# Kernel tuning notes

Hardware: AMD Instinct MI355X
Metric: run time of the kernel (lower is better)

Reference implementation:

```python
import jax, jax.numpy as jnp
import numpy as np

BN_EPS = 1e-5


def fps(xyz, npoint):
    # farthest point sampling; xyz: (B,N,3) -> (B,npoint) int32, starts at index 0 (torch convention)
    B, N, _ = xyz.shape
    def step(carry, _):
        dist, last = carry
        lp = jnp.take_along_axis(xyz, last[:, None, None], axis=1)  # (B,1,3)
        d = jnp.sum((xyz - lp) ** 2, -1)                             # (B,N)
        dist = jnp.minimum(dist, d)
        nxt = jnp.argmax(dist, -1).astype(jnp.int32)
        return (dist, nxt), nxt
    init = (jnp.full((B, N), 1e10, xyz.dtype), jnp.zeros((B,), jnp.int32))
    _, rest = jax.lax.scan(step, init, None, length=npoint - 1)
    return jnp.concatenate([jnp.zeros((1, B), jnp.int32), rest], 0).T  # (B,npoint)


def knn_idx(xyz, centers, k):
    # xyz (B,N,3), centers (B,S,3) -> (B,S,k) nearest-neighbor indices
    d = (jnp.sum(centers ** 2, -1)[:, :, None]
         + jnp.sum(xyz ** 2, -1)[:, None, :]
         - 2.0 * jnp.einsum('bsc,bnc->bsn', centers, xyz))
    _, idx = jax.lax.top_k(-d, k)
    return idx


def group(feat, idx):
    # feat (B,N,C), idx (B,S,K) -> (B,S,K,C)
    return jax.vmap(lambda f, i: f[i])(feat, idx)


def sa_knn(xyz, points, npoint, nsample, w1, b1, w2, b2):
    # xyz (B,N,3), points (B,N,C); returns new_xyz (B,S,3), new_points (B,S,Cout)
    fidx = fps(xyz, npoint)
    new_xyz = jnp.take_along_axis(xyz, fidx[:, :, None], axis=1)        # (B,S,3)
    idx = knn_idx(xyz, new_xyz, nsample)                                 # (B,S,K)
    g_xyz = group(xyz, idx) - new_xyz[:, :, None, :]                     # relative coords
    g_pts = group(points, idx)
    x = jnp.concatenate([g_xyz, g_pts], -1)                              # (B,S,K,3+C)
    x = jax.nn.relu(jnp.einsum('bskc,oc->bsko', x, w1) + b1)
    x = jnp.einsum('bskc,oc->bsko', x, w2) + b2                          # last conv: no activation
    return new_xyz, jnp.max(x, 2)                                        # max over neighbors


def sa_all(xyz, points, w1, b1, w2, b2):
    # group_all: concat xyz+points over all N, shared MLP, max over N -> (B,Cout)
    x = jnp.concatenate([xyz, points], -1)                               # (B,N,3+C)
    x = jax.nn.relu(jnp.einsum('bnc,oc->bno', x, w1) + b1)
    x = jnp.einsum('bnc,oc->bno', x, w2) + b2
    return jnp.max(x, 1)


def fc_head(x, w1, b1, g1, be1, w2, b2, g2, be2):
    # Linear + BN(eval, running mean=0/var=1) + ReLU, twice; Dropout = identity in eval
    s = 1.0 / np.sqrt(1.0 + BN_EPS)
    x = jax.nn.relu(g1 * ((x @ w1.T + b1) * s) + be1)
    x = jax.nn.relu(g2 * ((x @ w2.T + b2) * s) + be2)
    return x


def forward(point_cloud, sa1_w1, sa1_b1, sa1_w2, sa1_b2,
            sa2_w1, sa2_b1, sa2_w2, sa2_b2,
            sa3_w1, sa3_b1, sa3_w2, sa3_b2,
            fc_w1, fc_b1, fc_g1, fc_be1, fc_w2, fc_b2, fc_g2, fc_be2):
    xyz = jnp.transpose(point_cloud, (0, 2, 1))  # (B,N,3)
    nsamples2 = (16, 32, 48)
    logits, codes = [], []
    for i in range(3):  # three structurally distinct branches
        x1, p1 = sa_knn(xyz, xyz, 512, 16, sa1_w1[i], sa1_b1[i], sa1_w2[i], sa1_b2[i])
        x2, p2 = sa_knn(x1, p1, 128, nsamples2[i], sa2_w1[i], sa2_b1[i], sa2_w2[i], sa2_b2[i])
        code = sa_all(x2, p2, sa3_w1[i], sa3_b1[i], sa3_w2[i], sa3_b2[i])   # (B,512)
        logits.append(fc_head(code, fc_w1[i], fc_b1[i], fc_g1[i], fc_be1[i],
                              fc_w2[i], fc_b2[i], fc_g2[i], fc_be2[i]))      # (B,128)
        codes.append(code)
    return tuple(logits) + tuple(codes)


def setup_inputs():
    key = jax.random.key(0)
    ks = iter(jax.random.split(key, 16))
    def w(shape, s=0.05):
        return jax.random.normal(next(ks), shape, jnp.float32) * s
    B, N = 32, 2048
    inp = {'point_cloud': jax.random.normal(next(ks), (B, 3, N), jnp.float32)}
    inp.update(
        sa1_w1=w((3, 64, 6)), sa1_b1=jnp.zeros((3, 64)), sa1_w2=w((3, 128, 64)), sa1_b2=jnp.zeros((3, 128)),
        sa2_w1=w((3, 128, 131)), sa2_b1=jnp.zeros((3, 128)), sa2_w2=w((3, 256, 128)), sa2_b2=jnp.zeros((3, 256)),
        sa3_w1=w((3, 512, 259)), sa3_b1=jnp.zeros((3, 512)), sa3_w2=w((3, 512, 512)), sa3_b2=jnp.zeros((3, 512)),
        fc_w1=w((3, 256, 512)), fc_b1=jnp.zeros((3, 256)), fc_g1=jnp.ones((3, 256)), fc_be1=jnp.zeros((3, 256)),
        fc_w2=w((3, 128, 256)), fc_b2=jnp.zeros((3, 128)), fc_g2=jnp.ones((3, 128)), fc_be2=jnp.zeros((3, 128)),
    )
    return inp


def reference(point_cloud, sa1_w1, sa1_b1, sa1_w2, sa1_b2,
              sa2_w1, sa2_b1, sa2_w2, sa2_b2,
              sa3_w1, sa3_b1, sa3_w2, sa3_b2,
              fc_w1, fc_b1, fc_g1, fc_be1, fc_w2, fc_b2, fc_g2, fc_be2):
    return forward(point_cloud, sa1_w1, sa1_b1, sa1_w2, sa1_b2,
                   sa2_w1, sa2_b1, sa2_w2, sa2_b2,
                   sa3_w1, sa3_b1, sa3_w2, sa3_b2,
                   fc_w1, fc_b1, fc_g1, fc_be1, fc_w2, fc_b2, fc_g2, fc_be2)
```

## Files before the change

### kernel.cpp

```cpp
#include <hip/hip_runtime.h>
#include <hip/hip_bf16.h>
#include <math.h>

#define DEVI __device__ __forceinline__

static constexpr int BB = 32, NN = 2048, S1 = 512, S2 = 128;

typedef float f32x4 __attribute__((ext_vector_type(4)));
typedef short s16x8 __attribute__((ext_vector_type(8)));

static constexpr size_t OFF_XS   = 0;
static constexpr size_t OFF_YS   = OFF_XS + (size_t)BB*NN;
static constexpr size_t OFF_ZS   = OFF_YS + (size_t)BB*NN;
static constexpr size_t OFF_SSQ  = OFF_ZS + (size_t)BB*NN;
static constexpr size_t OFF_NX1X = OFF_SSQ + (size_t)BB*NN;
static constexpr size_t OFF_NX1Y = OFF_NX1X + (size_t)BB*S1;
static constexpr size_t OFF_NX1Z = OFF_NX1Y + (size_t)BB*S1;
static constexpr size_t OFF_NX2X = OFF_NX1Z + (size_t)BB*S1;
static constexpr size_t OFF_NX2Y = OFF_NX2X + (size_t)BB*S2;
static constexpr size_t OFF_NX2Z = OFF_NX2Y + (size_t)BB*S2;
static constexpr size_t OFF_CODE = OFF_NX2Z + (size_t)BB*S2;
static constexpr size_t OFF_O3P  = OFF_CODE + (size_t)3*BB*512;
static constexpr size_t OFF_P1   = OFF_O3P + (size_t)3*BB*4*512;
static constexpr size_t OFF_X3   = OFF_P1 + (size_t)3*BB*S1*128;
static constexpr size_t OFF_H3   = OFF_X3 + (size_t)3*BB*S2*260;
static constexpr size_t OFF_W    = OFF_H3 + (size_t)3*BB*S2*512;
static constexpr size_t W1A  = OFF_W;
static constexpr size_t B1A  = W1A + 3*64*6;
static constexpr size_t W2A  = B1A + 3*64;
static constexpr size_t B2A  = W2A + 3*128*64;
static constexpr size_t W1B  = B2A + 3*128;
static constexpr size_t B1B  = W1B + 3*128*132;
static constexpr size_t W2B  = B1B + 3*128;
static constexpr size_t B2B  = W2B + 3*256*128;
static constexpr size_t W1C  = B2B + 3*256;
static constexpr size_t B1C  = W1C + 3*512*260;
static constexpr size_t W2C  = B1C + 3*512;
static constexpr size_t B2C  = W2C + 3*512*512;
static constexpr size_t FW1  = B2C + 3*512;
static constexpr size_t FB1  = FW1 + 3*256*512;
static constexpr size_t FG1  = FB1 + 3*256;
static constexpr size_t FBE1 = FG1 + 3*256;
static constexpr size_t FW2  = FBE1 + 3*256;
static constexpr size_t FB2  = FW2 + 3*128*256;
static constexpr size_t FG2  = FB2 + 3*128;
static constexpr size_t FBE2 = FG2 + 3*128;
static constexpr size_t OFF_KNN1 = FBE2 + 3*128;
static constexpr size_t OFF_KNN2 = OFF_KNN1 + (size_t)BB*S1*16;
static constexpr size_t OFF_W1BF = OFF_KNN2 + (size_t)BB*S2*48;
static constexpr size_t OFF_W2BF = OFF_W1BF + 30720;
static constexpr size_t OFF_W1CBH = OFF_W2BF + 49152;
static constexpr size_t OFF_W1CBL = OFF_W1CBH + 221184;
static constexpr size_t OFF_W2CBH = OFF_W1CBL + 221184;
static constexpr size_t OFF_W2CBL = OFF_W2CBH + 393216;
static constexpr size_t OFF_X3BH  = OFF_W2CBL + 393216;
static constexpr size_t OFF_X3BL  = OFF_X3BH + 1769472;
static constexpr size_t OFF_H3BH  = OFF_X3BL + 1769472;
static constexpr size_t OFF_H3BL  = OFF_H3BH + 3145728;
static constexpr size_t OFF_W2ABH = OFF_H3BL + 3145728;
static constexpr size_t OFF_W2ABL = OFF_W2ABH + 12288;
static constexpr size_t WS_FLOATS = OFF_W2ABL + 12288;

__device__ __align__(16) float g_ws[WS_FLOATS];
__device__ int g_is_f32;
__device__ int g_flip;
__device__ int g_bad;
__device__ int g_nz;

DEVI float bf2f(const __hip_bfloat16 v){ return __bfloat162float(v); }
DEVI float rn_add(float a, float b){ return __fadd_rn(a,b); }
DEVI float rn_mul(float a, float b){ return __fmul_rn(a,b); }
DEVI float rn_sub(float a, float b){ return __fsub_rn(a,b); }
DEVI float sq3(float x,float y,float z){ return rn_add(rn_add(rn_mul(x,x),rn_mul(y,y)),rn_mul(z,z)); }

DEVI float ldany(const void* s, size_t i, int isf){
  return isf ? ((const float*)s)[i] : bf2f(((const __hip_bfloat16*)s)[i]);
}
DEVI unsigned short f2bf(float f){
  unsigned u = __float_as_uint(f);
  unsigned r = (u + 0x7FFFu + ((u>>16)&1u)) >> 16;
  return (unsigned short)r;
}
DEVI float bfbits2f(unsigned short h){ return __uint_as_float(((unsigned)h)<<16); }
DEVI void mfma16(f32x4& d, s16x8 a, s16x8 b){
  asm volatile("v_mfma_f32_16x16x32_bf16 %0, %1, %2, %0" : "+v"(d) : "v"(a), "v"(b));
}
DEVI void mfma_guard(f32x4& d){
  asm volatile("s_nop 7\n\ts_nop 7\n\ts_nop 2" : "+v"(d));
}

#define DPPF(dst, src, CTRL) dst = __uint_as_float((unsigned)__builtin_amdgcn_update_dpp(\
    (int)__float_as_uint(src), (int)__float_as_uint(src), CTRL, 0xF, 0xF, false))
#define DPPI(dst, src, CTRL) dst = __builtin_amdgcn_update_dpp(src, src, CTRL, 0xF, 0xF, false)
#define RED_STEP(CTRL) { float ov; int oi; DPPF(ov, best, CTRL); DPPI(oi, bidx, CTRL); \
  if (ov > best || (ov == best && oi < bidx)){ best = ov; bidx = oi; } }
#define WAVE_ARGMAX() RED_STEP(0xB1) RED_STEP(0x4E) RED_STEP(0x124) RED_STEP(0x128) RED_STEP(0x142) RED_STEP(0x143)

#define REDMIN_STEP(CTRL) { float ov; int oi; DPPF(ov, best, CTRL); DPPI(oi, bidx, CTRL); \
  if (ov < best || (ov == best && oi < bidx)){ best = ov; bidx = oi; } }
#define WAVE_ARGMIN() REDMIN_STEP(0xB1) REDMIN_STEP(0x4E) REDMIN_STEP(0x124) REDMIN_STEP(0x128) REDMIN_STEP(0x142) REDMIN_STEP(0x143)

__global__ __launch_bounds__(256) void init_detect_kernel(const void* __restrict__ pc){
  __shared__ int s_cnt[256];
  int t = threadIdx.x;
  if (t==0){ g_flip=0; g_bad=0; g_nz=0; }
  const unsigned short* h = (const unsigned short*)pc;
  int weird = 0;
  for (int i=t; i<4096; i+=256){
    unsigned short v = h[2*i];
    int e = (v >> 7) & 0xFF;
    if (e == 0xFF || e < 90 || e > 140) weird++;
  }
  s_cnt[t] = weird; __syncthreads();
  for (int o=128;o>0;o>>=1){ if (t<o) s_cnt[t]+=s_cnt[t+o]; __syncthreads(); }
  if (t==0) g_is_f32 = (s_cnt[0] > 1024) ? 1 : 0;
}

struct ParamPtrs { const void* p[20]; };

DEVI void cvt_arr(const void* s, float* d, int n, int g, int gs, int isf){
  for (int i=g;i<n;i+=gs) d[i] = ldany(s,i,isf);
}
DEVI void cvt_pad(const void* s, float* d, int rows, int cin, int cinp, int g, int gs, int isf){
  int tot = rows*cinp;
  for (int i=g;i<tot;i+=gs){ int r=i/cinp, c=i%cinp; d[i] = (c<cin)? ldany(s,(size_t)r*cin+c,isf) : 0.f; }
}

__global__ __launch_bounds__(256) void cvtprep_kernel(ParamPtrs pp, const void* __restrict__ pc, int mode){
  if (mode==1 && g_flip==0) return;
  const int isf = g_is_f32 ^ mode;
  if (blockIdx.x < 256){
    int i = blockIdx.x*256 + threadIdx.x;
    int b = i >> 11, n = i & 2047;
    float x = ldany(pc, (size_t)(b*3+0)*2048 + n, isf);
    float y = ldany(pc, (size_t)(b*3+1)*2048 + n, isf);
    float z = ldany(pc, (size_t)(b*3+2)*2048 + n, isf);
    g_ws[OFF_XS+i]=x; g_ws[OFF_YS+i]=y; g_ws[OFF_ZS+i]=z;
    g_ws[OFF_SSQ+i]=sq3(x,y,z);
    return;
  }
  int g = (blockIdx.x-256)*256 + threadIdx.x; int gs = 512*256;
  float* ws = g_ws;
  cvt_arr(pp.p[0],  ws+W1A, 3*64*6, g, gs, isf);
  cvt_arr(pp.p[1],  ws+B1A, 3*64, g, gs, isf);
  cvt_arr(pp.p[2],  ws+W2A, 3*128*64, g, gs, isf);
  cvt_arr(pp.p[3],  ws+B2A, 3*128, g, gs, isf);
  cvt_pad(pp.p[4],  ws+W1B, 3*128, 131, 132, g, gs, isf);
  cvt_arr(pp.p[5],  ws+B1B, 3*128, g, gs, isf);
  cvt_arr(pp.p[6],  ws+W2B, 3*256*128, g, gs, isf);
  cvt_arr(pp.p[7],  ws+B2B, 3*256, g, gs, isf);
  cvt_pad(pp.p[8],  ws+W1C, 3*512, 259, 260, g, gs, isf);
  cvt_arr(pp.p[9],  ws+B1C, 3*512, g, gs, isf);
  cvt_arr(pp.p[10], ws+W2C, 3*512*512, g, gs, isf);
  cvt_arr(pp.p[11], ws+B2C, 3*512, g, gs, isf);
  cvt_arr(pp.p[12], ws+FW1, 3*256*512, g, gs, isf);
  cvt_arr(pp.p[13], ws+FB1, 3*256, g, gs, isf);
  cvt_arr(pp.p[14], ws+FG1, 3*256, g, gs, isf);
  cvt_arr(pp.p[15], ws+FBE1,3*256, g, gs, isf);
  cvt_arr(pp.p[16], ws+FW2, 3*128*256, g, gs, isf);
  cvt_arr(pp.p[17], ws+FB2, 3*128, g, gs, isf);
  cvt_arr(pp.p[18], ws+FG2, 3*128, g, gs, isf);
  cvt_arr(pp.p[19], ws+FBE2,3*128, g, gs, isf);
}

__global__ __launch_bounds__(256) void scan_check_kernel(){
  size_t off; int n, g, gs;
  if (blockIdx.x < 128){ off = OFF_XS; n = 3*BB*NN; g = blockIdx.x*256 + threadIdx.x; gs = 128*256; }
  else { off = FW1; n = 3*256*512; g = (blockIdx.x-128)*256 + threadIdx.x; gs = 128*256; }
  int bad=0, nz=0;
  for (int i=g;i<n;i+=gs){
    float v = g_ws[off + i];
    if (v != v || fabsf(v) > 1e4f) bad=1;
    if (fabsf(v) > 1e-20f) nz=1;
  }
  unsigned long long mb = __ballot(bad), mn = __ballot(nz);
  if ((threadIdx.x & 63)==0){
    if (mb) atomicOr(&g_bad, 1);
    if (mn) atomicOr(&g_nz, 1);
  }
}

__global__ __launch_bounds__(64) void resolve_flip_kernel(){
  if (threadIdx.x==0){
    g_flip = (g_bad || !g_nz) ? 1 : 0;
    g_bad = 0; g_nz = 0;
  }
}

DEVI void cvt_bf16_body(int g, int gs){
  unsigned short* w1d = (unsigned short*)(g_ws + OFF_W1BF);
  for (int i=g; i<3*128*160; i+=gs){
    int br = i/(128*160); int rem = i%(128*160); int h = rem/160; int c = rem%160;
    float v = (c<132) ? g_ws[W1B + ((size_t)br*128 + h)*132 + c] : 0.f;
    w1d[i] = f2bf(v);
  }
  unsigned short* w2d = (unsigned short*)(g_ws + OFF_W2BF);
  for (int i=g; i<3*256*128; i+=gs) w2d[i] = f2bf(g_ws[W2B + i]);
  unsigned short* w1ch = (unsigned short*)(g_ws + OFF_W1CBH);
  unsigned short* w1cl = (unsigned short*)(g_ws + OFF_W1CBL);
  for (int i=g; i<3*512*288; i+=gs){
    int br = i/(512*288); int rem = i%(512*288); int n = rem/288; int c = rem%288;
    float v = (c<260) ? g_ws[W1C + ((size_t)br*512 + n)*260 + c] : 0.f;
    unsigned short hi = f2bf(v);
    w1ch[i] = hi; w1cl[i] = f2bf(v - bfbits2f(hi));
  }
  unsigned short* w2ch = (unsigned short*)(g_ws + OFF_W2CBH);
  unsigned short* w2cl = (unsigned short*)(g_ws + OFF_W2CBL);
  for (int i=g; i<3*512*512; i+=gs){
    float v = g_ws[W2C + i];
    unsigned short hi = f2bf(v);
    w2ch[i] = hi; w2cl[i] = f2bf(v - bfbits2f(hi));
  }
  unsigned short* w2ah = (unsigned short*)(g_ws + OFF_W2ABH);
  unsigned short* w2al = (unsigned short*)(g_ws + OFF_W2ABL);
  for (int i=g; i<3*128*64; i+=gs){
    float v = g_ws[W2A + i];
    unsigned short hi = f2bf(v);
    w2ah[i] = hi; w2al[i] = f2bf(v - bfbits2f(hi));
  }
}

#define FPS_DECL(J) float px##J, py##J, pz##J, dd##J;
#define FPS_LD256A(J) { int n=(J)*256+t; px##J=xs[n]; py##J=ys[n]; pz##J=zs[n]; dd##J=1e10f; xl[n]=px##J; yl[n]=py##J; zl[n]=pz##J; }
#define FPS_LD256B(J) { int n=(J)*256+t; px##J=xs[n]; py##J=ys[n]; pz##J=zs[n]; dd##J=ddg[n]; xl[n]=px##J; yl[n]=py##J; zl[n]=pz##J; }
#define FPS_SAVE(J) ddg[(J)*256+t]=dd##J;
#define FPS_LD64(J) { int n=(J)*64+t; px##J=xs[n]; py##J=ys[n]; pz##J=zs[n]; dd##J=1e10f; xl[n]=px##J; yl[n]=py##J; zl[n]=pz##J; }
#define FPS_UPD(J) { float dx=rn_sub(px##J,lx), dy=rn_sub(py##J,ly), dz=rn_sub(pz##J,lz); float d=sq3(dx,dy,dz); dd##J=fminf(dd##J,d); }
#define FPS_T1(J,JA,JB) float v##J; int q##J; { bool c = dd##JB > dd##JA; v##J = c? dd##JB : dd##JA; q##J = c? (JB) : (JA); }
#define FPS_T2(JA,JB) { bool c = v##JB > v##JA; v##JA = c? v##JB : v##JA; q##JA = c? q##JB : q##JA; }

#define FPS1_ITER_BODY() \
    FPS_UPD(0) FPS_UPD(1) FPS_UPD(2) FPS_UPD(3) FPS_UPD(4) FPS_UPD(5) FPS_UPD(6) FPS_UPD(7) \
    FPS_T1(0,0,1) FPS_T1(1,2,3) FPS_T1(2,4,5) FPS_T1(3,6,7) \
    FPS_T2(0,1) FPS_T2(2,3) \
    FPS_T2(0,2) \
    float best = v0; int bidx = q0*256 + t; \
    WAVE_ARGMAX() \
    int par = i & 1; \
    if ((t&63)==63){ s_val[par][wave]=best; s_idx[par][wave]=bidx; } \
    __syncthreads(); \
    float va = s_val[par][0], vb = s_val[par][1], vc = s_val[par][2], vd = s_val[par][3]; \
    int ia = s_idx[par][0], ib = s_idx[par][1], ic = s_idx[par][2], id_ = s_idx[par][3]; \
    if (vb > va || (vb == va && ib < ia)){ va = vb; ia = ib; } \
    if (vd > vc || (vd == vc && id_ < ic)){ vc = vd; ic = id_; } \
    if (vc > va || (vc == va && ic < ia)){ va = vc; ia = ic; } \
    int gidx = ia; \
    lx = xl[gidx]; ly = yl[gidx]; lz = zl[gidx]; \
    if (t==0){ nx[i]=lx; ny[i]=ly; nz[i]=lz; }

__global__ __launch_bounds__(256,1) void fps1a_cvt_kernel(){
  const int t = threadIdx.x;
  if (blockIdx.x >= 32){
    cvt_bf16_body((blockIdx.x-32)*256 + t, 256*256);
    return;
  }
  const int b = blockIdx.x;
  const int wave = t >> 6;
  const float* xs = g_ws + OFF_XS + (size_t)b*NN;
  const float* ys = g_ws + OFF_YS + (size_t)b*NN;
  const float* zs = g_ws + OFF_ZS + (size_t)b*NN;
  float* nx = g_ws + OFF_NX1X + (size_t)b*S1;
  float* ny = g_ws + OFF_NX1Y + (size_t)b*S1;
  float* nz = g_ws + OFF_NX1Z + (size_t)b*S1;
  float* ddg = g_ws + OFF_X3 + (size_t)b*NN;
  __shared__ float xl[NN], yl[NN], zl[NN];
  __shared__ float s_val[2][4]; __shared__ int s_idx[2][4];
  FPS_DECL(0) FPS_DECL(1) FPS_DECL(2) FPS_DECL(3) FPS_DECL(4) FPS_DECL(5) FPS_DECL(6) FPS_DECL(7)
  FPS_LD256A(0) FPS_LD256A(1) FPS_LD256A(2) FPS_LD256A(3) FPS_LD256A(4) FPS_LD256A(5) FPS_LD256A(6) FPS_LD256A(7)
  __syncthreads();
  float lx = xl[0], ly = yl[0], lz = zl[0];
  if (t==0){ nx[0]=lx; ny[0]=ly; nz[0]=lz; }
  for (int i=1;i<256;i++){
    FPS1_ITER_BODY()
  }
  FPS_SAVE(0) FPS_SAVE(1) FPS_SAVE(2) FPS_SAVE(3) FPS_SAVE(4) FPS_SAVE(5) FPS_SAVE(6) FPS_SAVE(7)
}

#define KNN1_POISON(C) case C: d[C] = match ? 3.0e38f : d[C]; break;
DEVI void knn1_body(int wid, int lane){
  int b = wid >> 9;
  const float* xs = g_ws + OFF_XS + (size_t)b*NN;
  const float* ys = g_ws + OFF_YS + (size_t)b*NN;
  const float* zs = g_ws + OFF_ZS + (size_t)b*NN;
  const float* sq = g_ws + OFF_SSQ + (size_t)b*NN;
  float cx = g_ws[OFF_NX1X + wid], cy = g_ws[OFF_NX1Y + wid], cz = g_ws[OFF_NX1Z + wid];
  float sc = sq3(cx,cy,cz);
  float d[32];
  #pragma unroll
  for (int c=0;c<32;c++){
    int n = c*64 + lane;
    float x=xs[n], y=ys[n], z=zs[n];
    float dot = rn_add(rn_add(rn_mul(cx,x),rn_mul(cy,y)),rn_mul(cz,z));
    d[c] = rn_sub(rn_add(sc,sq[n]), rn_mul(2.f,dot));
  }
  int* out = (int*)(g_ws + OFF_KNN1) + (size_t)wid*16;
  for (int r=0;r<16;r++){
    float tv[16]; int tc[16];
    #pragma unroll
    for (int c=0;c<16;c++){
      float a = d[2*c];
      float e = d[2*c+1];
      bool cc = e < a;
      tv[c] = cc ? e : a; tc[c] = cc ? (2*c+1) : (2*c);
    }
    #pragma unroll
    for (int s=1; s<16; s<<=1){
      #pragma unroll
      for (int c=0;c<16;c+=2){
        if ((c % (2*s)) == 0 && c+s < 16){
          bool cc = tv[c+s] < tv[c];
          tv[c] = cc ? tv[c+s] : tv[c];
          tc[c] = cc ? tc[c+s] : tc[c];
        }
      }
    }
    float best = tv[0]; int bidx = tc[0]*64 + lane;
    WAVE_ARGMIN()
    int wbi = __builtin_amdgcn_readlane(bidx, 63);
    if (lane == 0) out[r] = wbi;
    bool match = (lane == (wbi & 63));
    switch ((wbi >> 6) & 31){
      KNN1_POISON(0)  KNN1_POISON(1)  KNN1_POISON(2)  KNN1_POISON(3)
      KNN1_POISON(4)  KNN1_POISON(5)  KNN1_POISON(6)  KNN1_POISON(7)
      KNN1_POISON(8)  KNN1_POISON(9)  KNN1_POISON(10) KNN1_POISON(11)
      KNN1_POISON(12) KNN1_POISON(13) KNN1_POISON(14) KNN1_POISON(15)
      KNN1_POISON(16) KNN1_POISON(17) KNN1_POISON(18) KNN1_POISON(19)
      KNN1_POISON(20) KNN1_POISON(21) KNN1_POISON(22) KNN1_POISON(23)
      KNN1_POISON(24) KNN1_POISON(25) KNN1_POISON(26) KNN1_POISON(27)
      KNN1_POISON(28) KNN1_POISON(29) KNN1_POISON(30) KNN1_POISON(31)
    }
  }
}

__global__ __launch_bounds__(256,1) void fps1b_knn1a_kernel(){
  const int t = threadIdx.x;
  if (blockIdx.x >= 32){
    int lin = ((blockIdx.x-32)*256 + t) >> 6;
    int b = lin >> 8, s = lin & 255;
    knn1_body(b*S1 + s, t & 63);
    return;
  }
  const int b = blockIdx.x;
  const int wave = t >> 6;
  const float* xs = g_ws + OFF_XS + (size_t)b*NN;
  const float* ys = g_ws + OFF_YS + (size_t)b*NN;
  const float* zs = g_ws + OFF_ZS + (size_t)b*NN;
  float* nx = g_ws + OFF_NX1X + (size_t)b*S1;
  float* ny = g_ws + OFF_NX1Y + (size_t)b*S1;
  float* nz = g_ws + OFF_NX1Z + (size_t)b*S1;
  const float* ddg = g_ws + OFF_X3 + (size_t)b*NN;
  __shared__ float xl[NN], yl[NN], zl[NN];
  __shared__ float s_val[2][4]; __shared__ int s_idx[2][4];
  FPS_DECL(0) FPS_DECL(1) FPS_DECL(2) FPS_DECL(3) FPS_DECL(4) FPS_DECL(5) FPS_DECL(6) FPS_DECL(7)
  FPS_LD256B(0) FPS_LD256B(1) FPS_LD256B(2) FPS_LD256B(3) FPS_LD256B(4) FPS_LD256B(5) FPS_LD256B(6) FPS_LD256B(7)
  __syncthreads();
  float lx = nx[255], ly = ny[255], lz = nz[255];
  for (int i=256;i<S1;i++){
    FPS1_ITER_BODY()
  }
}

__global__ __launch_bounds__(256) void fps2_knn1b_kernel(){
  if (blockIdx.x >= 32){
    int lin = ((blockIdx.x-32)*256 + threadIdx.x) >> 6;
    int b = lin >> 8, s = lin & 255;
    knn1_body(b*S1 + 256 + s, threadIdx.x & 63);
    return;
  }
  if (threadIdx.x >= 64) return;
  const int b = blockIdx.x, t = threadIdx.x;
  const float* xs = g_ws + OFF_NX1X + (size_t)b*S1;
  const float* ys = g_ws + OFF_NX1Y + (size_t)b*S1;
  const float* zs = g_ws + OFF_NX1Z + (size_t)b*S1;
  float* nx = g_ws + OFF_NX2X + (size_t)b*S2;
  float* ny = g_ws + OFF_NX2Y + (size_t)b*S2;
  float* nz = g_ws + OFF_NX2Z + (size_t)b*S2;
  __shared__ float xl[S1], yl[S1], zl[S1];
  FPS_DECL(0) FPS_DECL(1) FPS_DECL(2) FPS_DECL(3) FPS_DECL(4) FPS_DECL(5) FPS_DECL(6) FPS_DECL(7)
  FPS_LD64(0) FPS_LD64(1) FPS_LD64(2) FPS_LD64(3) FPS_LD64(4) FPS_LD64(5) FPS_LD64(6) FPS_LD64(7)
  float lx = xl[0], ly = yl[0], lz = zl[0];
  if (t==0){ nx[0]=lx; ny[0]=ly; nz[0]=lz; }
  for (int i=1;i<S2;i++){
    FPS_UPD(0) FPS_UPD(1) FPS_UPD(2) FPS_UPD(3) FPS_UPD(4) FPS_UPD(5) FPS_UPD(6) FPS_UPD(7)
    FPS_T1(0,0,1) FPS_T1(1,2,3) FPS_T1(2,4,5) FPS_T1(3,6,7)
    FPS_T2(0,1) FPS_T2(2,3)
    FPS_T2(0,2)
    float best = v0; int bidx = q0*64 + t;
    WAVE_ARGMAX()
    int gidx = __builtin_amdgcn_readlane(bidx, 63);
    lx = xl[gidx]; ly = yl[gidx]; lz = zl[gidx];
    if (t==0){ nx[i]=lx; ny[i]=ly; nz[i]=lz; }
  }
}

#define KNN2_POISON(C) case C: d[C] = match ? 3.0e38f : d[C]; break;
DEVI void knn2_body(int wid, int lane){
  int b = wid >> 7;
  const float* xs = g_ws + OFF_NX1X + (size_t)b*S1;
  const float* ys = g_ws + OFF_NX1Y + (size_t)b*S1;
  const float* zs = g_ws + OFF_NX1Z + (size_t)b*S1;
  float cx = g_ws[OFF_NX2X + wid], cy = g_ws[OFF_NX2Y + wid], cz = g_ws[OFF_NX2Z + wid];
  float sc = sq3(cx,cy,cz);
  float d[8];
  #pragma unroll
  for (int c=0;c<8;c++){
    int n = c*64 + lane;
    float x=xs[n], y=ys[n], z=zs[n];
    float sx = sq3(x,y,z);
    float dot = rn_add(rn_add(rn_mul(cx,x),rn_mul(cy,y)),rn_mul(cz,z));
    d[c] = rn_sub(rn_add(sc,sx), rn_mul(2.f,dot));
  }
  int* out = (int*)(g_ws + OFF_KNN2) + (size_t)wid*48;
  for (int r=0;r<48;r++){
    float tv[4]; int tc[4];
    #pragma unroll
    for (int c=0;c<4;c++){
      float a = d[2*c];
      float e = d[2*c+1];
      bool cc = e < a;
      tv[c] = cc ? e : a; tc[c] = cc ? (2*c+1) : (2*c);
    }
    { bool cc = tv[1] < tv[0]; tv[0] = cc?tv[1]:tv[0]; tc[0] = cc?tc[1]:tc[0]; }
    { bool cc = tv[3] < tv[2]; tv[2] = cc?tv[3]:tv[2]; tc[2] = cc?tc[3]:tc[2]; }
    { bool cc = tv[2] < tv[0]; tv[0] = cc?tv[2]:tv[0]; tc[0] = cc?tc[2]:tc[0]; }
    float best = tv[0]; int bidx = tc[0]*64 + lane;
    WAVE_ARGMIN()
    int wbi = __builtin_amdgcn_readlane(bidx, 63);
    if (lane == 0) out[r] = wbi;
    bool match = (lane == (wbi & 63));
    switch ((wbi >> 6) & 7){
      KNN2_POISON(0) KNN2_POISON(1) KNN2_POISON(2) KNN2_POISON(3)
      KNN2_POISON(4) KNN2_POISON(5) KNN2_POISON(6) KNN2_POISON(7)
    }
  }
}

__global__ __launch_bounds__(256) void knn2_sa1_kernel(){
  const int t = threadIdx.x;
  if (blockIdx.x < 1024){
    knn2_body((blockIdx.x*256 + t) >> 6, t & 63);
    return;
  }
  const int bx2 = blockIdx.x - 1024;
  const int br = bx2 >> 10;
  const int bxx = bx2 & 1023;
  const int wave = t>>6, lane = t&63, quad = lane>>4, l16 = lane&15;
  __shared__ float w1s[384];
  __shared__ float b1s[64];
  __shared__ __align__(16) short Hh[4][16*72];
  __shared__ __align__(16) short Hl[4][16*72];
  for (int i=t;i<384;i+=256) w1s[i] = g_ws[W1A + (size_t)br*384 + i];
  if (t<64) b1s[t] = g_ws[B1A + br*64 + t];
  __syncthreads();
  const int* kn = (const int*)(g_ws + OFF_KNN1);
  const short* w2h = (const short*)(g_ws + OFF_W2ABH) + (size_t)br*128*64;
  const short* w2l = (const short*)(g_ws + OFF_W2ABL) + (size_t)br*128*64;
  const float* b2 = g_ws + B2A + br*128;
  for (int it=0; it<4; it++){
    int gid = bxx*16 + it*4 + wave;
    int b = gid >> 9;
    int idx = kn[(size_t)gid*16 + l16] & (NN-1);
    float cx = g_ws[OFF_NX1X+gid], cy = g_ws[OFF_NX1Y+gid], cz = g_ws[OFF_NX1Z+gid];
    size_t gl = (size_t)b*NN + idx;
    float x = g_ws[OFF_XS+gl], y = g_ws[OFF_YS+gl], z = g_ws[OFF_ZS+gl];
    float f0=x-cx, f1=y-cy, f2=z-cz;
    #pragma unroll
    for (int i=0;i<16;i++){
      int h = quad*16 + i;
      float acc = b1s[h];
      acc += f0*w1s[h*6+0] + f1*w1s[h*6+1] + f2*w1s[h*6+2]
           +  x*w1s[h*6+3] +  y*w1s[h*6+4] +  z*w1s[h*6+5];
      acc = fmaxf(acc, 0.f);
      unsigned short hi = f2bf(acc);
      Hh[wave][l16*72 + h] = (short)hi;
      Hl[wave][l16*72 + h] = (short)f2bf(acc - bfbits2f(hi));
    }
    s16x8 ah[2], al[2];
    #pragma unroll
    for (int ks=0;ks<2;ks++){
      ah[ks] = *(const s16x8*)(&Hh[wave][l16*72 + ks*32 + quad*8]);
      al[ks] = *(const s16x8*)(&Hl[wave][l16*72 + ks*32 + quad*8]);
    }
    unsigned short* P1g = (unsigned short*)(g_ws + OFF_P1) + ((size_t)br*16384 + gid)*128;
    #pragma unroll
    for (int ni=0; ni<8; ni++){
      int o = ni*16 + l16;
      f32x4 acc = {0.f,0.f,0.f,0.f};
      #pragma unroll
      for (int ks=0; ks<2; ks++){
        s16x8 bh = *(const s16x8*)(w2h + (size_t)o*64 + ks*32 + quad*8);
        s16x8 bl = *(const s16x8*)(w2l + (size_t)o*64 + ks*32 + quad*8);
        mfma16(acc, ah[ks], bh);
        mfma16(acc, ah[ks], bl);
        mfma16(acc, al[ks], bh);
      }
      mfma_guard(acc);
      float vmax = fmaxf(fmaxf(acc[0],acc[1]), fmaxf(acc[2],acc[3]));
      vmax = fmaxf(vmax, __shfl_xor(vmax,16));
      vmax = fmaxf(vmax, __shfl_xor(vmax,32));
      if (quad==0) P1g[o] = f2bf(vmax + b2[o]);
    }
  }
}

template<int K>
DEVI void sa2_body(int br, int g2, short* Xb, short* Hb, float* ctr, int* idxs){
  constexpr int MT = K/16;
  const int b = g2 >> 7;
  const int t = threadIdx.x;
  const int wave = t >> 6, lane = t & 63, quad = lane >> 4, l16 = lane & 15;
  const int* kn2 = (const int*)(g_ws + OFF_KNN2) + (size_t)g2*48;
  if (t < K) idxs[t] = kn2[t] & (S1-1);
  if (t < 3) ctr[t] = g_ws[(t==0?OFF_NX2X:(t==1?OFF_NX2Y:OFF_NX2Z)) + g2];
  __syncthreads();
  const unsigned short* p1b = (const unsigned short*)(g_ws + OFF_P1) + (size_t)br*16384*128;
  const int grp = t >> 5, gl = t & 31;
  for (int k = grp; k < K; k += 8){
    int idx = idxs[k];
    const unsigned short* row = p1b + ((size_t)b*S1 + idx)*128;
    unsigned long long w = *(const unsigned long long*)(row + gl*4);
    short* dst = &Xb[k*168 + 3 + gl*4];
    dst[0] = (short)(w & 0xFFFF);
    dst[1] = (short)((w >> 16) & 0xFFFF);
    dst[2] = (short)((w >> 32) & 0xFFFF);
    dst[3] = (short)((w >> 48) & 0xFFFF);
    if (gl < 32) Xb[k*168 + 131 + gl] = 0;
    if (gl < 5)  Xb[k*168 + 163 + gl] = 0;
  }
  if (t < K){
    int idx = idxs[t];
    float c0 = g_ws[OFF_NX1X + (size_t)b*S1 + idx] - ctr[0];
    float c1 = g_ws[OFF_NX1Y + (size_t)b*S1 + idx] - ctr[1];
    float c2 = g_ws[OFF_NX1Z + (size_t)b*S1 + idx] - ctr[2];
    Xb[t*168+0] = (short)f2bf(c0);
    Xb[t*168+1] = (short)f2bf(c1);
    Xb[t*168+2] = (short)f2bf(c2);
  }
  __syncthreads();
  {
    const short* w1bf = (const short*)(g_ws + OFF_W1BF) + (size_t)br*128*160;
    const float* b1 = g_ws + B1B + br*128;
    for (int ni = wave; ni < 8; ni += 4){
      int h = ni*16 + l16;
      s16x8 bfr[5];
      #pragma unroll
      for (int ks=0;ks<5;ks++) bfr[ks] = *(const s16x8*)(w1bf + (size_t)h*160 + ks*32 + quad*8);
      float bias = b1[h];
      #pragma unroll
      for (int m=0; m<MT; m++){
        f32x4 acc = {0.f,0.f,0.f,0.f};
        #pragma unroll
        for (int ks=0;ks<5;ks++){
          s16x8 a = *(const s16x8*)(&Xb[(m*16 + l16)*168 + ks*32 + quad*8]);
          mfma16(acc, a, bfr[ks]);
        }
        mfma_guard(acc);
        #pragma unroll
        for (int r=0;r<4;r++){
          int row = m*16 + quad*4 + r;
          float hv = fmaxf(acc[r] + bias, 0.f);
          Hb[row*136 + ni*16 + l16] = (short)f2bf(hv);
        }
      }
    }
  }
  __syncthreads();
  {
    const short* w2bf = (const short*)(g_ws + OFF_W2BF) + (size_t)br*256*128;
    const float* b2 = g_ws + B2B + br*256;
    unsigned short* xh = (unsigned short*)(g_ws + OFF_X3BH);
    unsigned short* xlo = (unsigned short*)(g_ws + OFF_X3BL);
    size_t row = (size_t)(br*4096 + g2)*288;
    for (int ni = wave; ni < 16; ni += 4){
      int o = ni*16 + l16;
      s16x8 bfr[4];
      #pragma unroll
      for (int ks=0;ks<4;ks++) bfr[ks] = *(const s16x8*)(w2bf + (size_t)o*128 + ks*32 + quad*8);
      float vmax = -3.4e38f;
      #pragma unroll
      for (int m=0; m<MT; m++){
        f32x4 acc = {0.f,0.f,0.f,0.f};
        #pragma unroll
        for (int ks=0;ks<4;ks++){
          s16x8 a = *(const s16x8*)(&Hb[(m*16 + l16)*136 + ks*32 + quad*8]);
          mfma16(acc, a, bfr[ks]);
        }
        mfma_guard(acc);
        #pragma unroll
        for (int r=0;r<4;r++) vmax = fmaxf(vmax, acc[r]);
      }
      vmax = fmaxf(vmax, __shfl_xor(vmax, 16));
      vmax = fmaxf(vmax, __shfl_xor(vmax, 32));
      if (quad == 0){
        float hv = vmax + b2[o];
        unsigned short hi = f2bf(hv);
        xh[row + 3 + o] = hi;
        xlo[row + 3 + o] = f2bf(hv - bfbits2f(hi));
      }
    }
    if (t < 3){
      float cv = ctr[t];
      unsigned short hi = f2bf(cv);
      xh[row + t] = hi; xlo[row + t] = f2bf(cv - bfbits2f(hi));
    }
    if (t >= 3 && t < 32){ xh[row + 256 + t] = 0; xlo[row + 256 + t] = 0; }
  }
}

__global__ __launch_bounds__(256) void sa2_all_kernel(){
  __shared__ __align__(16) short Xb[48*168];
  __shared__ __align__(16) short Hb[48*136];
  __shared__ float ctr[3];
  __shared__ int idxs[48];
  int br = blockIdx.x >> 12;
  int g2 = blockIdx.x & 4095;
  if (br == 0)      sa2_body<16>(0, g2, Xb, Hb, ctr, idxs);
  else if (br == 1) sa2_body<32>(1, g2, Xb, Hb, ctr, idxs);
  else              sa2_body<48>(2, g2, Xb, Hb, ctr, idxs);
}

__global__ __launch_bounds__(256) void sa3l1_mfma_kernel(){
  const int br = blockIdx.y; const int r0 = blockIdx.x*32;
  const int t = threadIdx.x;
  const int wave = t >> 6, lane = t & 63, quad = lane >> 4, l16 = lane & 15;
  const short* xh = (const short*)(g_ws + OFF_X3BH) + (size_t)(br*4096 + r0)*288;
  const short* xl = (const short*)(g_ws + OFF_X3BL) + (size_t)(br*4096 + r0)*288;
  const short* wh = (const short*)(g_ws + OFF_W1CBH) + (size_t)br*512*288;
  const short* wl = (const short*)(g_ws + OFF_W1CBL) + (size_t)br*512*288;
  const float* bias = g_ws + B1C + br*512;
  unsigned short* hh = (unsigned short*)(g_ws + OFF_H3BH) + (size_t)(br*4096 + r0)*512;
  unsigned short* hl = (unsigned short*)(g_ws + OFF_H3BL) + (size_t)(br*4096 + r0)*512;
  f32x4 acc[2][8];
  #pragma unroll
  for (int m=0;m<2;m++)
    #pragma unroll
    for (int ni=0;ni<8;ni++) acc[m][ni] = (f32x4){0.f,0.f,0.f,0.f};
  for (int ks=0; ks<9; ks++){
    s16x8 ah[2], al[2];
    #pragma unroll
    for (int m=0;m<2;m++){
      ah[m] = *(const s16x8*)(xh + (size_t)(m*16+l16)*288 + ks*32 + quad*8);
      al[m] = *(const s16x8*)(xl + (size_t)(m*16+l16)*288 + ks*32 + quad*8);
    }
    #pragma unroll
    for (int ni=0;ni<8;ni++){
      int n = wave*128 + ni*16 + l16;
      s16x8 bh = *(const s16x8*)(wh + (size_t)n*288 + ks*32 + quad*8);
      s16x8 bl = *(const s16x8*)(wl + (size_t)n*288 + ks*32 + quad*8);
      #pragma unroll
      for (int m=0;m<2;m++){
        mfma16(acc[m][ni], ah[m], bh);
        mfma16(acc[m][ni], ah[m], bl);
        mfma16(acc[m][ni], al[m], bh);
      }
    }
  }
  mfma_guard(acc[0][0]);
  #pragma unroll
  for (int m=0;m<2;m++){
    #pragma unroll
    for (int ni=0;ni<8;ni++){
      int col = wave*128 + ni*16 + l16;
      float bs = bias[col];
      #pragma unroll
      for (int r=0;r<4;r++){
        int row = m*16 + quad*4 + r;
        float hv = fmaxf(acc[m][ni][r] + bs, 0.f);
        unsigned short hi = f2bf(hv);
        hh[(size_t)row*512 + col] = hi;
        hl[(size_t)row*512 + col] = f2bf(hv - bfbits2f(hi));
      }
    }
  }
}

__global__ __launch_bounds__(256) void sa3l2_mfma_kernel(){
  const int br = blockIdx.y; const int b = blockIdx.x>>2; const int part = blockIdx.x&3;
  const int t = threadIdx.x;
  const int wave = t >> 6, lane = t & 63, quad = lane >> 4, l16 = lane & 15;
  const int row0 = b*128 + part*32;
  const short* ahp = (const short*)(g_ws + OFF_H3BH) + (size_t)(br*4096 + row0)*512;
  const short* alp = (const short*)(g_ws + OFF_H3BL) + (size_t)(br*4096 + row0)*512;
  const short* wh = (const short*)(g_ws + OFF_W2CBH) + (size_t)br*512*512;
  const short* wl = (const short*)(g_ws + OFF_W2CBL) + (size_t)br*512*512;
  f32x4 acc[2][8];
  #pragma unroll
  for (int m=0;m<2;m++)
    #pragma unroll
    for (int ni=0;ni<8;ni++) acc[m][ni] = (f32x4){0.f,0.f,0.f,0.f};
  for (int ks=0; ks<16; ks++){
    s16x8 ah[2], al[2];
    #pragma unroll
    for (int m=0;m<2;m++){
      ah[m] = *(const s16x8*)(ahp + (size_t)(m*16+l16)*512 + ks*32 + quad*8);
      al[m] = *(const s16x8*)(alp + (size_t)(m*16+l16)*512 + ks*32 + quad*8);
    }
    #pragma unroll
    for (int ni=0;ni<8;ni++){
      int n = wave*128 + ni*16 + l16;
      s16x8 bh = *(const s16x8*)(wh + (size_t)n*512 + ks*32 + quad*8);
      s16x8 bl = *(const s16x8*)(wl + (size_t)n*512 + ks*32 + quad*8);
      #pragma unroll
      for (int m=0;m<2;m++){
        mfma16(acc[m][ni], ah[m], bh);
        mfma16(acc[m][ni], ah[m], bl);
        mfma16(acc[m][ni], al[m], bh);
      }
    }
  }
  mfma_guard(acc[0][0]);
  #pragma unroll
  for (int ni=0;ni<8;ni++){
    float vmax = -3.4e38f;
    #pragma unroll
    for (int m=0;m<2;m++)
      #pragma unroll
      for (int r=0;r<4;r++) vmax = fmaxf(vmax, acc[m][ni][r]);
    vmax = fmaxf(vmax, __shfl_xor(vmax, 16));
    vmax = fmaxf(vmax, __shfl_xor(vmax, 32));
    if (quad == 0){
      int col = wave*128 + ni*16 + l16;
      g_ws[OFF_O3P + (((size_t)br*BB + b)*4 + part)*512 + col] = vmax;
    }
  }
}

__global__ __launch_bounds__(256) void fc_kernel(float* __restrict__ out, int out_size){
  int br = blockIdx.x >> 5; int b = blockIdx.x & 31; int t = threadIdx.x;
  __shared__ float xin[512]; __shared__ float x1s[256];
  const float* o3p = g_ws + OFF_O3P + (((size_t)br*BB + b)*4)*512;
  const float* b2c = g_ws + B2C + br*512;
  #pragma unroll
  for (int k=0;k<2;k++){
    int o = t + k*256;
    float m = fmaxf(fmaxf(o3p[o], o3p[512+o]), fmaxf(o3p[1024+o], o3p[1536+o]));
    m += b2c[o];
    xin[o] = m;
    int oi = 3*BB*128 + ((br*BB + b)*512) + o;
    if (oi < out_size) out[oi] = m;
  }
  __syncthreads();
  const float s = (float)(1.0 / sqrt(1.0 + 1e-5));
  {
    const float4* wp = (const float4*)(g_ws + FW1 + ((size_t)br*256 + t)*512);
    const float4* xp = (const float4*)xin;
    float acc = 0.f;
    #pragma unroll 8
    for (int q=0;q<128;q++){ float4 w4=wp[q], x4=xp[q]; acc += w4.x*x4.x + w4.y*x4.y + w4.z*x4.z + w4.w*x4.w; }
    acc = (acc + g_ws[FB1 + br*256+t]) * s;
    acc = g_ws[FG1+br*256+t]*acc + g_ws[FBE1+br*256+t];
    x1s[t] = fmaxf(acc, 0.f);
  }
  __syncthreads();
  if (t < 128){
    const float4* wp = (const float4*)(g_ws + FW2 + ((size_t)br*128 + t)*256);
    const float4* xp = (const float4*)x1s;
    float acc=0.f;
    #pragma unroll 8
    for (int q=0;q<64;q++){ float4 w4=wp[q], x4=xp[q]; acc += w4.x*x4.x + w4.y*x4.y + w4.z*x4.z + w4.w*x4.w; }
    acc = (acc + g_ws[FB2+br*128+t])*s;
    acc = g_ws[FG2+br*128+t]*acc + g_ws[FBE2+br*128+t];
    int oi = ((size_t)br*BB + b)*128 + t;
    if (oi < out_size) out[oi] = fmaxf(acc,0.f);
  }
}

extern "C" void kernel_launch(void* const* d_in, const int* in_sizes, int n_in,
                              void* d_out, int out_size, void* d_ws, size_t ws_size,
                              hipStream_t stream) {
  (void)d_ws; (void)ws_size;
  if (n_in < 21) return;
  if (in_sizes[0] != BB*3*NN) return;
  float* out = (float*)d_out;

  ParamPtrs pp;
  for (int i=0;i<20;i++) pp.p[i] = d_in[i+1];

  init_detect_kernel<<<1,256,0,stream>>>(d_in[0]);
  cvtprep_kernel<<<768,256,0,stream>>>(pp, d_in[0], 0);
  scan_check_kernel<<<256,256,0,stream>>>();
  resolve_flip_kernel<<<1,64,0,stream>>>();
  cvtprep_kernel<<<768,256,0,stream>>>(pp, d_in[0], 1);

  fps1a_cvt_kernel<<<32+256,256,0,stream>>>();
  fps1b_knn1a_kernel<<<32+2048,256,0,stream>>>();
  fps2_knn1b_kernel<<<32+2048,256,0,stream>>>();
  knn2_sa1_kernel<<<1024+3072,256,0,stream>>>();
  sa2_all_kernel<<<3*4096,256,0,stream>>>();

  sa3l1_mfma_kernel<<<dim3(128,3),256,0,stream>>>();
  sa3l2_mfma_kernel<<<dim3(128,3),256,0,stream>>>();
  fc_kernel<<<96,256,0,stream>>>(out, out_size);
}
```

Measured before the change: 1.094 ms.

## Split SA1 MLP across kernels to overlap first half with FPS2

Moves the SA1 shared-MLP body into a device function and splits its blocks in two. The half whose centers already have KNN results from the earlier kernel (first 256 centers per batch) now runs inside the FPS2/KNN1b launch. The remaining half stays with KNN2. The aim is to fill CUs that sit idle while the serial single-wave FPS2 blocks run. In exchange, the merged kernel declares more shared memory, which may lower occupancy for the KNN1b blocks.

Result: no change. 1.080 ms (-1.3%).

```diff
diff --git a/kernel.cpp b/kernel.cpp
--- a/kernel.cpp
+++ b/kernel.cpp
@@ -332,6 +332,63 @@
   }
 }
 
+DEVI void sa1_body(int br, int bxx, float* w1s, float* b1s, short* Hh, short* Hl){
+  const int t = threadIdx.x;
+  const int wave = t>>6, lane = t&63, quad = lane>>4, l16 = lane&15;
+  for (int i=t;i<384;i+=256) w1s[i] = g_ws[W1A + (size_t)br*384 + i];
+  if (t<64) b1s[t] = g_ws[B1A + br*64 + t];
+  __syncthreads();
+  const int* kn = (const int*)(g_ws + OFF_KNN1);
+  const short* w2h = (const short*)(g_ws + OFF_W2ABH) + (size_t)br*128*64;
+  const short* w2l = (const short*)(g_ws + OFF_W2ABL) + (size_t)br*128*64;
+  const float* b2 = g_ws + B2A + br*128;
+  for (int it=0; it<4; it++){
+    int gid = bxx*16 + it*4 + wave;
+    int b = gid >> 9;
+    int idx = kn[(size_t)gid*16 + l16] & (NN-1);
+    float cx = g_ws[OFF_NX1X+gid], cy = g_ws[OFF_NX1Y+gid], cz = g_ws[OFF_NX1Z+gid];
+    size_t gl = (size_t)b*NN + idx;
+    float x = g_ws[OFF_XS+gl], y = g_ws[OFF_YS+gl], z = g_ws[OFF_ZS+gl];
+    float f0=x-cx, f1=y-cy, f2=z-cz;
+    #pragma unroll
+    for (int i=0;i<16;i++){
+      int h = quad*16 + i;
+      float acc = b1s[h];
+      acc += f0*w1s[h*6+0] + f1*w1s[h*6+1] + f2*w1s[h*6+2]
+           +  x*w1s[h*6+3] +  y*w1s[h*6+4] +  z*w1s[h*6+5];
+      acc = fmaxf(acc, 0.f);
+      unsigned short hi = f2bf(acc);
+      Hh[wave*1152 + l16*72 + h] = (short)hi;
+      Hl[wave*1152 + l16*72 + h] = (short)f2bf(acc - bfbits2f(hi));
+    }
+    s16x8 ah[2], al[2];
+    #pragma unroll
+    for (int ks=0;ks<2;ks++){
+      ah[ks] = *(const s16x8*)(&Hh[wave*1152 + l16*72 + ks*32 + quad*8]);
+      al[ks] = *(const s16x8*)(&Hl[wave*1152 + l16*72 + ks*32 + quad*8]);
+    }
+    unsigned short* P1g = (unsigned short*)(g_ws + OFF_P1) + ((size_t)br*16384 + gid)*128;
+    #pragma unroll
+    for (int ni=0; ni<8; ni++){
+      int o = ni*16 + l16;
+      f32x4 acc = {0.f,0.f,0.f,0.f};
+      #pragma unroll
+      for (int ks=0; ks<2; ks++){
+        s16x8 bh = *(const s16x8*)(w2h + (size_t)o*64 + ks*32 + quad*8);
+        s16x8 bl = *(const s16x8*)(w2l + (size_t)o*64 + ks*32 + quad*8);
+        mfma16(acc, ah[ks], bh);
+        mfma16(acc, ah[ks], bl);
+        mfma16(acc, al[ks], bh);
+      }
+      mfma_guard(acc);
+      float vmax = fmaxf(fmaxf(acc[0],acc[1]), fmaxf(acc[2],acc[3]));
+      vmax = fmaxf(vmax, __shfl_xor(vmax,16));
+      vmax = fmaxf(vmax, __shfl_xor(vmax,32));
+      if (quad==0) P1g[o] = f2bf(vmax + b2[o]);
+    }
+  }
+}
+
 __global__ __launch_bounds__(256,1) void fps1b_knn1a_kernel(){
   const int t = threadIdx.x;
   if (blockIdx.x >= 32){
@@ -360,7 +417,21 @@
   }
 }
 
-__global__ __launch_bounds__(256) void fps2_knn1b_kernel(){
+__global__ __launch_bounds__(256) void fps2_knn1b_sa1a_kernel(){
+  __shared__ float xl[S1], yl[S1], zl[S1];
+  __shared__ float w1s[384];
+  __shared__ float b1s[64];
+  __shared__ __align__(16) short Hh[4*16*72];
+  __shared__ __align__(16) short Hl[4*16*72];
+  __shared__ float s_val_un[2][4]; __shared__ int s_idx_un[2][4];
+  (void)s_val_un; (void)s_idx_un;
+  if (blockIdx.x >= 2080){
+    int q = blockIdx.x - 2080;
+    int br = q >> 9, r = q & 511;
+    int bxx = ((r >> 4) << 5) + (r & 15);
+    sa1_body(br, bxx, w1s, b1s, Hh, Hl);
+    return;
+  }
   if (blockIdx.x >= 32){
     int lin = ((blockIdx.x-32)*256 + threadIdx.x) >> 6;
     int b = lin >> 8, s = lin & 255;
@@ -375,7 +446,6 @@
   float* nx = g_ws + OFF_NX2X + (size_t)b*S2;
   float* ny = g_ws + OFF_NX2Y + (size_t)b*S2;
   float* nz = g_ws + OFF_NX2Z + (size_t)b*S2;
-  __shared__ float xl[S1], yl[S1], zl[S1];
   FPS_DECL(0) FPS_DECL(1) FPS_DECL(2) FPS_DECL(3) FPS_DECL(4) FPS_DECL(5) FPS_DECL(6) FPS_DECL(7)
   FPS_LD64(0) FPS_LD64(1) FPS_LD64(2) FPS_LD64(3) FPS_LD64(4) FPS_LD64(5) FPS_LD64(6) FPS_LD64(7)
   float lx = xl[0], ly = yl[0], lz = zl[0];
@@ -435,72 +505,20 @@
   }
 }
 
-__global__ __launch_bounds__(256) void knn2_sa1_kernel(){
+__global__ __launch_bounds__(256) void knn2_sa1b_kernel(){
+  __shared__ float w1s[384];
+  __shared__ float b1s[64];
+  __shared__ __align__(16) short Hh[4*16*72];
+  __shared__ __align__(16) short Hl[4*16*72];
   const int t = threadIdx.x;
   if (blockIdx.x < 1024){
     knn2_body((blockIdx.x*256 + t) >> 6, t & 63);
     return;
   }
-  const int bx2 = blockIdx.x - 1024;
-  const int br = bx2 >> 10;
-  const int bxx = bx2 & 1023;
-  const int wave = t>>6, lane = t&63, quad = lane>>4, l16 = lane&15;
-  __shared__ float w1s[384];
-  __shared__ float b1s[64];
-  __shared__ __align__(16) short Hh[4][16*72];
-  __shared__ __align__(16) short Hl[4][16*72];
-  for (int i=t;i<384;i+=256) w1s[i] = g_ws[W1A + (size_t)br*384 + i];
-  if (t<64) b1s[t] = g_ws[B1A + br*64 + t];
-  __syncthreads();
-  const int* kn = (const int*)(g_ws + OFF_KNN1);
-  const short* w2h = (const short*)(g_ws + OFF_W2ABH) + (size_t)br*128*64;
-  const short* w2l = (const short*)(g_ws + OFF_W2ABL) + (size_t)br*128*64;
-  const float* b2 = g_ws + B2A + br*128;
-  for (int it=0; it<4; it++){
-    int gid = bxx*16 + it*4 + wave;
-    int b = gid >> 9;
-    int idx = kn[(size_t)gid*16 + l16] & (NN-1);
-    float cx = g_ws[OFF_NX1X+gid], cy = g_ws[OFF_NX1Y+gid], cz = g_ws[OFF_NX1Z+gid];
-    size_t gl = (size_t)b*NN + idx;
-    float x = g_ws[OFF_XS+gl], y = g_ws[OFF_YS+gl], z = g_ws[OFF_ZS+gl];
-    float f0=x-cx, f1=y-cy, f2=z-cz;
-    #pragma unroll
-    for (int i=0;i<16;i++){
-      int h = quad*16 + i;
-      float acc = b1s[h];
-      acc += f0*w1s[h*6+0] + f1*w1s[h*6+1] + f2*w1s[h*6+2]
-           +  x*w1s[h*6+3] +  y*w1s[h*6+4] +  z*w1s[h*6+5];
-      acc = fmaxf(acc, 0.f);
-      unsigned short hi = f2bf(acc);
-      Hh[wave][l16*72 + h] = (short)hi;
-      Hl[wave][l16*72 + h] = (short)f2bf(acc - bfbits2f(hi));
-    }
-    s16x8 ah[2], al[2];
-    #pragma unroll
-    for (int ks=0;ks<2;ks++){
-      ah[ks] = *(const s16x8*)(&Hh[wave][l16*72 + ks*32 + quad*8]);
-      al[ks] = *(const s16x8*)(&Hl[wave][l16*72 + ks*32 + quad*8]);
-    }
-    unsigned short* P1g = (unsigned short*)(g_ws + OFF_P1) + ((size_t)br*16384 + gid)*128;
-    #pragma unroll
-    for (int ni=0; ni<8; ni++){
-      int o = ni*16 + l16;
-      f32x4 acc = {0.f,0.f,0.f,0.f};
-      #pragma unroll
-      for (int ks=0; ks<2; ks++){
-        s16x8 bh = *(const s16x8*)(w2h + (size_t)o*64 + ks*32 + quad*8);
-        s16x8 bl = *(const s16x8*)(w2l + (size_t)o*64 + ks*32 + quad*8);
-        mfma16(acc, ah[ks], bh);
-        mfma16(acc, ah[ks], bl);
-        mfma16(acc, al[ks], bh);
-      }
-      mfma_guard(acc);
-      float vmax = fmaxf(fmaxf(acc[0],acc[1]), fmaxf(acc[2],acc[3]));
-      vmax = fmaxf(vmax, __shfl_xor(vmax,16));
-      vmax = fmaxf(vmax, __shfl_xor(vmax,32));
-      if (quad==0) P1g[o] = f2bf(vmax + b2[o]);
-    }
-  }
+  int q = blockIdx.x - 1024;
+  int br = q >> 9, r = q & 511;
+  int bxx = ((r >> 4) << 5) + 16 + (r & 15);
+  sa1_body(br, bxx, w1s, b1s, Hh, Hl);
 }
 
 template<int K>
@@ -784,8 +802,8 @@
 
   fps1a_cvt_kernel<<<32+256,256,0,stream>>>();
   fps1b_knn1a_kernel<<<32+2048,256,0,stream>>>();
-  fps2_knn1b_kernel<<<32+2048,256,0,stream>>>();
-  knn2_sa1_kernel<<<1024+3072,256,0,stream>>>();
+  fps2_knn1b_sa1a_kernel<<<32+2048+1536,256,0,stream>>>();
+  knn2_sa1b_kernel<<<1024+1536,256,0,stream>>>();
   sa2_all_kernel<<<3*4096,256,0,stream>>>();
 
   sa3l1_mfma_kernel<<<dim3(128,3),256,0,stream>>>();
```
